# Optimization experiments

Hardware: AMD Instinct MI355X
Metric: run time of the kernel (lower is better)

## Reference

```python
import jax, jax.numpy as jnp
import numpy as np
from jax import lax

DN = ('NHWC', 'HWIO', 'NHWC')

def conv2d_same(x, W, b):
    y = lax.conv_general_dilated(x, W, window_strides=(1, 1), padding='SAME', dimension_numbers=DN)
    return y + b

def maxpool2(x):
    # 2x2 max pool, stride 2, SAME padding (NHWC)
    return lax.reduce_window(x, -jnp.inf, lax.max, (1, 2, 2, 1), (1, 2, 2, 1), 'SAME')

def setup_inputs() -> dict:
    key = jax.random.key(0)
    ks = jax.random.split(key, 6)
    B, H, W, C = 8, 64, 64, 256
    s = 0.05
    return {
        'x': jax.random.normal(ks[0], (B, H, W, C), jnp.float32),
        'Wf': jax.random.normal(ks[1], (3, 3, C, C // 8), jnp.float32) * s,
        'bf': jnp.zeros((C // 8,), jnp.float32),
        'Wg': jax.random.normal(ks[2], (3, 3, C, C // 8), jnp.float32) * s,
        'bg': jnp.zeros((C // 8,), jnp.float32),
        'Wh': jax.random.normal(ks[3], (3, 3, C, C // 2), jnp.float32) * s,
        'bh': jnp.zeros((C // 2,), jnp.float32),
        'Wo': jax.random.normal(ks[4], (1, 1, C // 2, C), jnp.float32) * s,
        'bo': jnp.zeros((C,), jnp.float32),
        'gate': jnp.ones((1,), jnp.float32),
    }

def reference(x, Wf, bf, Wg, bg, Wh, bh, Wo, bo, gate):
    B, H, W, C = x.shape
    f = maxpool2(conv2d_same(x, Wf, bf))            # [B, H/2, W/2, C//8] keys
    g = conv2d_same(x, Wg, bg)                       # [B, H, W, C//8]     queries
    h = maxpool2(conv2d_same(x, Wh, bh))            # [B, H/2, W/2, C//2] values
    N, M = H * W, (H // 2) * (W // 2)
    gq = g.reshape(B, N, C // 8)
    fk = f.reshape(B, M, C // 8)
    hv = h.reshape(B, M, C // 2)
    attn = jax.nn.softmax(jnp.einsum('bnd,bmd->bnm', gq, fk), axis=-1)  # [B, N, M]
    wo = jnp.einsum('bnm,bmv->bnv', attn, hv).reshape(B, H, W, C // 2)
    out = conv2d_same(wo, Wo, bo)                    # [B, H, W, C]
    return x + gate[0] * out
```

## Files before the change

kernel.cpp:

```cpp
#include <hip/hip_runtime.h>
#include <hip/hip_fp16.h>

constexpr int B_  = 8;
constexpr int H_  = 64;
constexpr int W_  = 64;
constexpr int C_  = 256;
constexpr int CG_ = 32;
constexpr int CH_ = 128;
constexpr int NQ_ = 4096;
constexpr int NM_ = 1024;

constexpr int GP_ = 1048576;
constexpr int HP_ = 4194304;

typedef __attribute__((ext_vector_type(8))) _Float16 half8;
typedef __attribute__((ext_vector_type(4))) _Float16 half4;
typedef __attribute__((ext_vector_type(4))) float    f32x4;

__global__ void prep_w_k(const float* __restrict__ Wg, const float* __restrict__ Wf,
                         const float* __restrict__ Wh, const float* __restrict__ Wo,
                         const float* __restrict__ bg, const float* __restrict__ bf,
                         const float* __restrict__ bh,
                         _Float16* __restrict__ Wpk, _Float16* __restrict__ Wok,
                         float* __restrict__ bc) {
    int i = blockIdx.x * 256 + threadIdx.x;
    if (i < 12 * 9 * 8 * 64 * 8) {
        int j    = i & 7;
        int lane = (i >> 3) & 63;
        int ks   = (i >> 9) & 7;
        int tap  = (i >> 12) % 9;
        int co16 = i / 36864;
        int co = co16 * 16 + (lane & 15);
        int kk = tap * 256 + ks * 32 + (lane >> 4) * 8 + j;
        float v;
        if (co < 32)      v = Wg[(size_t)kk * 32  + co];
        else if (co < 64) v = Wf[(size_t)kk * 32  + (co - 32)];
        else              v = Wh[(size_t)kk * 128 + (co - 64)];
        Wpk[i] = (_Float16)v;
        return;
    }
    int i2 = i - 12 * 9 * 8 * 64 * 8;
    if (i2 < 16 * 4 * 64 * 8) {
        int j    = i2 & 7;
        int lane = (i2 >> 3) & 63;
        int ks   = (i2 >> 9) & 3;
        int co16 = i2 >> 11;
        int co = co16 * 16 + (lane & 15);
        int k  = ks * 32 + (lane >> 4) * 8 + j;
        Wok[i2] = (_Float16)Wo[(size_t)k * 256 + co];
        return;
    }
    int co = i2 - 16 * 4 * 64 * 8;
    if (co < 192)
        bc[co] = (co < 32) ? bg[co] : (co < 64) ? bf[co - 32] : bh[co - 64];
}

__global__ __launch_bounds__(512, 4) void conv_mfma_k(
        const float* __restrict__ X, const _Float16* __restrict__ Wpk,
        const float* __restrict__ bc,
        _Float16* __restrict__ gpart, _Float16* __restrict__ fpart,
        _Float16* __restrict__ hpart) {
    __shared__ char lds[2 * 32768];
    int bid = blockIdx.x;
    int lg  = (bid & 7) * 96 + (bid >> 3);
    int ky  = lg % 3;
    int ip  = lg / 3;
    int b   = ip >> 5;
    int y0  = (ip & 31) * 2;
    int tid = threadIdx.x;
    int wid = tid >> 6;
    int rid = wid >> 2;
    int nw  = wid & 3;
    int l   = tid & 63;
    int lr  = l & 15;
    int lk  = l >> 4;

    {
#pragma unroll
        for (int j = 0; j < 8; ++j) {
            int cc  = tid + j * 512;
            int row = cc >> 11;
            int c   = cc & 2047;
            int px  = c >> 5;
            int c8  = (c & 31) * 8;
            int yin = y0 + ky - 1 + row;
            half8 v = (half8)(_Float16)0.f;
            if (yin >= 0 && yin < 64) {
                const float* s = X + (((size_t)(b * 64 + yin) * 64) + px) * 256 + c8;
                float4 a  = *reinterpret_cast<const float4*>(s);
                float4 b2 = *reinterpret_cast<const float4*>(s + 4);
                v[0] = (_Float16)a.x;  v[1] = (_Float16)a.y;
                v[2] = (_Float16)a.z;  v[3] = (_Float16)a.w;
                v[4] = (_Float16)b2.x; v[5] = (_Float16)b2.y;
                v[6] = (_Float16)b2.z; v[7] = (_Float16)b2.w;
            }
            *reinterpret_cast<half8*>(lds + row * 32768 +
                ((c * 16) ^ ((px & 7) << 4))) = v;
        }
    }
    __syncthreads();

    f32x4 acc[4][3];
#pragma unroll
    for (int mi = 0; mi < 4; ++mi)
#pragma unroll
        for (int nj = 0; nj < 3; ++nj) acc[mi][nj] = (f32x4)0.f;

    int tap0 = ky * 3;
    const char* ldsr = lds + rid * 32768;

    auto ldw = [&](int s, half8* d) {
        const _Float16* p = Wpk +
            ((((size_t)(nw * 3) * 9 + tap0 + (s >> 3)) * 8 + (s & 7)) * 64 + l) * 8;
        d[0] = *reinterpret_cast<const half8*>(p);
        d[1] = *reinterpret_cast<const half8*>(p + 36864);
        d[2] = *reinterpret_cast<const half8*>(p + 73728);
    };
    auto lda = [&](int s, half8* d) {
        int kx = s >> 3, ks = s & 7;
#pragma unroll
        for (int mi = 0; mi < 4; ++mi) {
            int px  = mi * 16 + lr + kx - 1;
            int pxc = px < 0 ? 0 : (px > 63 ? 63 : px);
            int ad  = (pxc * 512 + ks * 64 + lk * 16) ^ ((pxc & 7) << 4);
            half8 a = *reinterpret_cast<const half8*>(ldsr + ad);
            if (px < 0 || px > 63) a = (half8)(_Float16)0.f;
            d[mi] = a;
        }
    };

    half8 wb[2][3];
    half8 afb[2][4];
    ldw(0, wb[0]);
    lda(0, afb[0]);
#pragma unroll
    for (int st = 0; st < 24; ++st) {
        if (st < 23) {
            ldw(st + 1, wb[(st + 1) & 1]);
            lda(st + 1, afb[(st + 1) & 1]);
        }
        const half8* w  = wb[st & 1];
        const half8* af = afb[st & 1];
        __builtin_amdgcn_s_setprio(1);
#pragma unroll
        for (int mi = 0; mi < 4; ++mi)
            acc[mi][0] = __builtin_amdgcn_mfma_f32_16x16x32_f16(af[mi], w[0], acc[mi][0], 0, 0, 0);
#pragma unroll
        for (int mi = 0; mi < 4; ++mi)
            acc[mi][1] = __builtin_amdgcn_mfma_f32_16x16x32_f16(af[mi], w[1], acc[mi][1], 0, 0, 0);
#pragma unroll
        for (int mi = 0; mi < 4; ++mi)
            acc[mi][2] = __builtin_amdgcn_mfma_f32_16x16x32_f16(af[mi], w[2], acc[mi][2], 0, 0, 0);
        __builtin_amdgcn_s_setprio(0);
    }

    int pixbase = (b * 64 + y0 + rid) * 64;
    bool addb = (ky == 1);
#pragma unroll
    for (int nj = 0; nj < 3; ++nj) {
        int co = nw * 48 + nj * 16 + lr;
        float bias = addb ? bc[co] : 0.f;
#pragma unroll
        for (int mi = 0; mi < 4; ++mi) {
#pragma unroll
            for (int r = 0; r < 4; ++r) {
                int x = mi * 16 + lk * 4 + r;
                float v = acc[mi][nj][r] + bias;
                size_t pix = pixbase + x;
                if (co < 32)
                    gpart[(size_t)ky * GP_ + pix * 32 + co] = (_Float16)(v * 1.44269504f);
                else if (co < 64)
                    fpart[(size_t)ky * GP_ + pix * 32 + (co - 32)] = (_Float16)v;
                else
                    hpart[(size_t)ky * HP_ + pix * 128 + (co - 64)] = (_Float16)v;
            }
        }
    }
}

__global__ __launch_bounds__(256) void pools_k(const _Float16* __restrict__ fp,
                                               const _Float16* __restrict__ hp,
                                               _Float16* __restrict__ Kf,
                                               _Float16* __restrict__ Vt) {
    __shared__ float t[32][33];
    int blk = blockIdx.x;
    int tid = threadIdx.x;
    if (blk < 1024) {
        int i = blk * 256 + tid;
        int c = i & 31;
        int t2 = i >> 5;
        int px = t2 & 31;
        int py = (t2 >> 5) & 31;
        int b  = t2 >> 10;
        size_t base = (((size_t)(b * 64 + py * 2)) * 64 + px * 2) * 32 + c;
        const _Float16* p1 = fp + GP_;
        const _Float16* p2 = fp + 2 * GP_;
        auto val = [&](size_t o) { return (float)fp[o] + (float)p1[o] + (float)p2[o]; };
        float v = fmaxf(fmaxf(val(base), val(base + 32)),
                        fmaxf(val(base + 64 * 32), val(base + 64 * 32 + 32)));
        Kf[i] = (_Float16)v;
        return;
    }
    int bx = blk - 1024;
    int b  = bx >> 7;
    int kt = (bx >> 2) & 31;
    int ct = bx & 3;
    const _Float16* p1 = hp + HP_;
    const _Float16* p2 = hp + 2 * (size_t)HP_;
#pragma unroll
    for (int i = 0; i < 4; ++i) {
        int e = tid + i * 256;
        int px = e >> 5, c = e & 31;
        size_t base = (((size_t)(b * 64 + kt * 2) * 64) + px * 2) * 128 + ct * 32 + c;
        auto val = [&](size_t o) { return (float)hp[o] + (float)p1[o] + (float)p2[o]; };
        float v = fmaxf(fmaxf(val(base), val(base + 128)),
                        fmaxf(val(base + 64 * 128), val(base + 64 * 128 + 128)));
        t[px][c] = v;
    }
    __syncthreads();
#pragma unroll
    for (int i = 0; i < 4; ++i) {
        int e = tid + i * 256;
        int c = e >> 5, px = e & 31;
        Vt[((size_t)b * 128 + ct * 32 + c) * 1024 + kt * 32 + px] = (_Float16)t[px][c];
    }
}

constexpr int PP_ = 72;

__global__ __launch_bounds__(256, 2) void attn_flash_k(
        const _Float16* __restrict__ Qp,
        const _Float16* __restrict__ Kf,
        const _Float16* __restrict__ Vt,
        _Float16* __restrict__ wo) {
    __shared__ _Float16 plds[4][16][PP_];
    __shared__ _Float16 vlds[2][8192];
    int bb  = blockIdx.x >> 6;
    int qt  = blockIdx.x & 63;
    int wid = threadIdx.x >> 6;
    int l   = threadIdx.x & 63;
    int lr  = l & 15;
    int lg  = l >> 4;
    int qbase = qt * 64 + wid * 16;

    const _Float16* gp = Qp + ((size_t)bb * NQ_ + qbase + lr) * 32 + lg * 8;
    half8 bq = *reinterpret_cast<const half8*>(gp);
    bq = bq + *reinterpret_cast<const half8*>(gp + GP_);
    bq = bq + *reinterpret_cast<const half8*>(gp + 2 * GP_);

    const _Float16* Kb = Kf + (size_t)bb * NM_ * 32;
    const _Float16* Vb = Vt + (size_t)bb * 128 * NM_;

    int o0  = wid * 4096 + l * 16;
    int vr0 = o0 >> 7;
    int vc  = (o0 >> 4) & 7;
    int vsw = (vr0 & 7) << 4;
    int lsw = (lr & 7) << 4;

    f32x4 acc[8];
#pragma unroll
    for (int vt = 0; vt < 8; ++vt) acc[vt] = (f32x4)0.f;
    float m_run = -1.0e30f;
    float l_lane = 0.f;

    half8 ak0, ak1, ak2, ak3;
    f32x4 s0, s1, s2, s3;
    half4 ph0, ph1, ph2, ph3;
    float4 vst[4];

#define STAGE_LOAD(T)                                                              \
    {   const _Float16* vp = Vb + (size_t)(T) * 64 + (size_t)vr0 * NM_ + vc * 8;   \
        vst[0] = *reinterpret_cast<const float4*>(vp);                             \
        vst[1] = *reinterpret_cast<const float4*>(vp + 8 * NM_);                   \
        vst[2] = *reinterpret_cast<const float4*>(vp + 16 * NM_);                  \
        vst[3] = *reinterpret_cast<const float4*>(vp + 24 * NM_);                  \
    }

#define STAGE_WRITE(BUF)                                                           \
    {   char* vbp = (char*)vlds[BUF] + (o0 ^ vsw);                                 \
        *reinterpret_cast<float4*>(vbp)        = vst[0];                           \
        *reinterpret_cast<float4*>(vbp + 1024) = vst[1];                           \
        *reinterpret_cast<float4*>(vbp + 2048) = vst[2];                           \
        *reinterpret_cast<float4*>(vbp + 3072) = vst[3];                           \
    }

#define LOADK(T)                                                                   \
    {   const _Float16* kp = Kb + (size_t)(T) * 64 * 32;                           \
        ak0 = *reinterpret_cast<const half8*>(kp + (size_t)(lr)      * 32 + lg*8); \
        ak1 = *reinterpret_cast<const half8*>(kp + (size_t)(16 + lr) * 32 + lg*8); \
        ak2 = *reinterpret_cast<const half8*>(kp + (size_t)(32 + lr) * 32 + lg*8); \
        ak3 = *reinterpret_cast<const half8*>(kp + (size_t)(48 + lr) * 32 + lg*8); \
    }

#define QK()                                                                \
    {   __builtin_amdgcn_s_setprio(1);                                      \
        s0 = __builtin_amdgcn_mfma_f32_16x16x32_f16(ak0, bq, (f32x4)0.f, 0, 0, 0); \
        s1 = __builtin_amdgcn_mfma_f32_16x16x32_f16(ak1, bq, (f32x4)0.f, 0, 0, 0); \
        s2 = __builtin_amdgcn_mfma_f32_16x16x32_f16(ak2, bq, (f32x4)0.f, 0, 0, 0); \
        s3 = __builtin_amdgcn_mfma_f32_16x16x32_f16(ak3, bq, (f32x4)0.f, 0, 0, 0); \
        __builtin_amdgcn_s_setprio(0);                                      \
    }

#define SOFTMAX()                                                           \
    {   float lm = fmaxf(fmaxf(fmaxf(s0[0], s0[1]), fmaxf(s0[2], s0[3])),   \
                         fmaxf(fmaxf(s1[0], s1[1]), fmaxf(s1[2], s1[3])));  \
        lm = fmaxf(lm, fmaxf(fmaxf(fmaxf(s2[0], s2[1]), fmaxf(s2[2], s2[3])), \
                             fmaxf(fmaxf(s3[0], s3[1]), fmaxf(s3[2], s3[3])))); \
        if (__any(lm > m_run + 11.0f)) {                                    \
            float mx = lm;                                                  \
            mx = fmaxf(mx, __shfl_xor(mx, 16, 64));                         \
            mx = fmaxf(mx, __shfl_xor(mx, 32, 64));                         \
            float mnew  = fmaxf(m_run, mx);                                 \
            float alpha = exp2f(m_run - mnew);                              \
            l_lane *= alpha;                                                \
            _Pragma("unroll")                                               \
            for (int r = 0; r < 4; ++r) {                                   \
                float ar = __shfl(alpha, 4 * lg + r, 64);                   \
                _Pragma("unroll")                                           \
                for (int vt = 0; vt < 8; ++vt) acc[vt][r] *= ar;            \
            }                                                               \
            m_run = mnew;                                                   \
        }                                                                   \
        float ps = 0.f;                                                     \
        {   float p0 = exp2f(s0[0]-m_run), p1 = exp2f(s0[1]-m_run);         \
            float p2 = exp2f(s0[2]-m_run), p3 = exp2f(s0[3]-m_run);         \
            ps += (p0+p1)+(p2+p3);                                          \
            ph0[0]=(_Float16)p0; ph0[1]=(_Float16)p1;                       \
            ph0[2]=(_Float16)p2; ph0[3]=(_Float16)p3; }                     \
        {   float p0 = exp2f(s1[0]-m_run), p1 = exp2f(s1[1]-m_run);         \
            float p2 = exp2f(s1[2]-m_run), p3 = exp2f(s1[3]-m_run);         \
            ps += (p0+p1)+(p2+p3);                                          \
            ph1[0]=(_Float16)p0; ph1[1]=(_Float16)p1;                       \
            ph1[2]=(_Float16)p2; ph1[3]=(_Float16)p3; }                     \
        {   float p0 = exp2f(s2[0]-m_run), p1 = exp2f(s2[1]-m_run);         \
            float p2 = exp2f(s2[2]-m_run), p3 = exp2f(s2[3]-m_run);         \
            ps += (p0+p1)+(p2+p3);                                          \
            ph2[0]=(_Float16)p0; ph2[1]=(_Float16)p1;                       \
            ph2[2]=(_Float16)p2; ph2[3]=(_Float16)p3; }                     \
        {   float p0 = exp2f(s3[0]-m_run), p1 = exp2f(s3[1]-m_run);         \
            float p2 = exp2f(s3[2]-m_run), p3 = exp2f(s3[3]-m_run);         \
            ps += (p0+p1)+(p2+p3);                                          \
            ph3[0]=(_Float16)p0; ph3[1]=(_Float16)p1;                       \
            ph3[2]=(_Float16)p2; ph3[3]=(_Float16)p3; }                     \
        l_lane += ps;                                                       \
    }

#define WRITEP()                                                            \
    {   *reinterpret_cast<half4*>(&plds[wid][lr][ 0 + 4*lg]) = ph0;         \
        *reinterpret_cast<half4*>(&plds[wid][lr][16 + 4*lg]) = ph1;         \
        *reinterpret_cast<half4*>(&plds[wid][lr][32 + 4*lg]) = ph2;         \
        *reinterpret_cast<half4*>(&plds[wid][lr][48 + 4*lg]) = ph3;         \
    }

#define PV(BUF)                                                             \
    {   half8 ap0 = *reinterpret_cast<const half8*>(&plds[wid][lr][8*lg]);  \
        half8 ap1 = *reinterpret_cast<const half8*>(&plds[wid][lr][32 + 8*lg]); \
        const char* vbp = (const char*)vlds[BUF];                           \
        __builtin_amdgcn_s_setprio(1);                                      \
        _Pragma("unroll")                                                   \
        for (int vt = 0; vt < 8; ++vt) {                                    \
            int ra = (vt * 16 + lr) * 128;                                  \
            half8 bv = *reinterpret_cast<const half8*>(                     \
                vbp + ((ra + lg * 16) ^ lsw));                              \
            acc[vt] = __builtin_amdgcn_mfma_f32_16x16x32_f16(ap0, bv, acc[vt], 0, 0, 0); \
        }                                                                   \
        _Pragma("unroll")                                                   \
        for (int vt = 0; vt < 8; ++vt) {                                    \
            int ra = (vt * 16 + lr) * 128;                                  \
            half8 bv = *reinterpret_cast<const half8*>(                     \
                vbp + ((ra + (4 + lg) * 16) ^ lsw));                        \
            acc[vt] = __builtin_amdgcn_mfma_f32_16x16x32_f16(ap1, bv, acc[vt], 0, 0, 0); \
        }                                                                   \
        __builtin_amdgcn_s_setprio(0);                                      \
    }

    STAGE_LOAD(0);
    STAGE_WRITE(0);
    LOADK(0);
    __syncthreads();
    QK(); SOFTMAX();

    for (int t = 0; t < 16; ++t) {
        if (t < 15) { STAGE_LOAD(t + 1); LOADK(t + 1); }
        WRITEP();
        PV(t & 1);
        if (t < 15) STAGE_WRITE((t + 1) & 1);
        __syncthreads();
        if (t < 15) { QK(); SOFTMAX(); }
    }

#undef STAGE_LOAD
#undef STAGE_WRITE
#undef LOADK
#undef QK
#undef SOFTMAX
#undef WRITEP
#undef PV

    float lsum = l_lane;
    lsum += __shfl_xor(lsum, 16, 64);
    lsum += __shfl_xor(lsum, 32, 64);
    float inv = 1.f / lsum;
#pragma unroll
    for (int r = 0; r < 4; ++r) {
        float ir = __shfl(inv, 4 * lg + r, 64);
        _Float16* orow = wo + ((size_t)bb * NQ_ + qbase + 4 * lg + r) * 128 + lr;
#pragma unroll
        for (int vt = 0; vt < 8; ++vt) orow[vt * 16] = (_Float16)(acc[vt][r] * ir);
    }
}

__global__ __launch_bounds__(256, 2) void conv1x1_mfma_k(
        const _Float16* __restrict__ wo, const _Float16* __restrict__ Wok,
        const float* __restrict__ bo, const float* __restrict__ X,
        const float* __restrict__ gate, float* __restrict__ out) {
    __shared__ char lds[64 * 256];
    int pix0 = blockIdx.x * 64;
    int tid = threadIdx.x;
    int wq = tid >> 6;
    int l  = tid & 63;
    int lr = l & 15;
    int lg = l >> 4;

    {
        const float4* sp = reinterpret_cast<const float4*>(wo + (size_t)pix0 * 128);
#pragma unroll
        for (int j = 0; j < 4; ++j) {
            int c = tid + j * 256;
            int px = c >> 4;
            *reinterpret_cast<float4*>(lds + ((c * 16) ^ ((px & 7) << 4))) = sp[c];
        }
    }
    __syncthreads();

    f32x4 acc[4][4];
#pragma unroll
    for (int mi = 0; mi < 4; ++mi)
#pragma unroll
        for (int nj = 0; nj < 4; ++nj) acc[mi][nj] = (f32x4)0.f;

#pragma unroll
    for (int ks = 0; ks < 4; ++ks) {
        half8 ap[4];
#pragma unroll
        for (int mi = 0; mi < 4; ++mi) {
            int px = mi * 16 + lr;
            int ad = (px * 256 + ks * 64 + lg * 16) ^ ((px & 7) << 4);
            ap[mi] = *reinterpret_cast<const half8*>(lds + ad);
        }
#pragma unroll
        for (int nj = 0; nj < 4; ++nj) {
            int co16 = wq * 4 + nj;
            half8 bv = *reinterpret_cast<const half8*>(
                Wok + (((size_t)co16 * 4 + ks) * 64 + l) * 8);
#pragma unroll
            for (int mi = 0; mi < 4; ++mi)
                acc[mi][nj] = __builtin_amdgcn_mfma_f32_16x16x32_f16(ap[mi], bv, acc[mi][nj], 0, 0, 0);
        }
    }

    float gt = gate[0];
#pragma unroll
    for (int nj = 0; nj < 4; ++nj) {
        int co = wq * 64 + nj * 16 + lr;
        float bias = bo[co];
#pragma unroll
        for (int mi = 0; mi < 4; ++mi) {
#pragma unroll
            for (int r = 0; r < 4; ++r) {
                size_t o = (size_t)(pix0 + mi * 16 + lg * 4 + r) * 256 + co;
                out[o] = X[o] + gt * (acc[mi][nj][r] + bias);
            }
        }
    }
}

extern "C" void kernel_launch(void* const* d_in, const int* in_sizes, int n_in,
                              void* d_out, int out_size, void* d_ws, size_t ws_size,
                              hipStream_t stream) {
    const float* X    = (const float*)d_in[0];
    const float* Wf   = (const float*)d_in[1];
    const float* bf   = (const float*)d_in[2];
    const float* Wg   = (const float*)d_in[3];
    const float* bg   = (const float*)d_in[4];
    const float* Wh   = (const float*)d_in[5];
    const float* bh   = (const float*)d_in[6];
    const float* Wo   = (const float*)d_in[7];
    const float* bo   = (const float*)d_in[8];
    const float* gate = (const float*)d_in[9];
    float* out = (float*)d_out;

    _Float16* gpart = (_Float16*)d_ws;
    _Float16* fpart = gpart + 3 * (size_t)GP_;
    _Float16* hpart = fpart + 3 * (size_t)GP_;
    _Float16* Kf    = hpart + 3 * (size_t)HP_;
    _Float16* Vt    = Kf + 262144;
    _Float16* Wpk   = Vt + 1048576;
    float*    bc    = (float*)(Wpk + 442368);
    _Float16* Wok   = (_Float16*)(bc + 192);
    _Float16* wobuf = hpart;

    prep_w_k<<<(12*9*8*64*8 + 16*4*64*8 + 192 + 255) / 256, 256, 0, stream>>>(
        Wg, Wf, Wh, Wo, bg, bf, bh, Wpk, Wok, bc);
    conv_mfma_k<<<3 * B_ * 32, 512, 0, stream>>>(X, Wpk, bc, gpart, fpart, hpart);
    pools_k<<<2048, 256, 0, stream>>>(fpart, hpart, Kf, Vt);
    attn_flash_k<<<B_ * 64, 256, 0, stream>>>(gpart, Kf, Vt, wobuf);
    conv1x1_mfma_k<<<(B_ * NQ_) / 64, 256, 0, stream>>>(wobuf, Wok, bo, X, gate, out);
}
```

Before: 107.7 us.

## Pre-pad input to fp16 buffer and shrink conv tiles to half-row blocks

Adds a prep pass that converts X to a zero-padded fp16 NHWC buffer, so the conv kernel copies raw fp16 data into LDS without per-element conversion or boundary masking. The conv kernel now handles one half-row (32 pixels) per 256-thread block instead of two full rows per 512-thread block, with smaller LDS and accumulator footprint, four times as many blocks, and higher occupancy bounds. The explicit software double-buffering of weight and activation loads and the setprio hints are removed. The cost is an extra full pass writing and reading the padded fp16 copy of X, and each weight fragment is now reused across fewer pixels.

```diff
diff --git a/kernel.cpp b/kernel.cpp
--- a/kernel.cpp
+++ b/kernel.cpp
@@ -9,38 +9,65 @@
 constexpr int CH_ = 128;
 constexpr int NQ_ = 4096;
 constexpr int NM_ = 1024;
+constexpr int XP_ = 66;
 
 constexpr int GP_ = 1048576;
 constexpr int HP_ = 4194304;
+
+constexpr int NWPK_ = 12 * 9 * 8 * 64 * 8;
+constexpr int NWOK_ = 16 * 4 * 64 * 8;
+constexpr int NXC_  = B_ * XP_ * XP_ * 32;
 
 typedef __attribute__((ext_vector_type(8))) _Float16 half8;
 typedef __attribute__((ext_vector_type(4))) _Float16 half4;
 typedef __attribute__((ext_vector_type(4))) float    f32x4;
 
-__global__ void prep_w_k(const float* __restrict__ Wg, const float* __restrict__ Wf,
-                         const float* __restrict__ Wh, const float* __restrict__ Wo,
-                         const float* __restrict__ bg, const float* __restrict__ bf,
-                         const float* __restrict__ bh,
-                         _Float16* __restrict__ Wpk, _Float16* __restrict__ Wok,
-                         float* __restrict__ bc) {
+__global__ void prep_all_k(const float* __restrict__ X,
+                           const float* __restrict__ Wg, const float* __restrict__ Wf,
+                           const float* __restrict__ Wh, const float* __restrict__ Wo,
+                           const float* __restrict__ bg, const float* __restrict__ bf,
+                           const float* __restrict__ bh,
+                           _Float16* __restrict__ Xpad, _Float16* __restrict__ Wpk,
+                           _Float16* __restrict__ Wok, float* __restrict__ bc) {
     int i = blockIdx.x * 256 + threadIdx.x;
-    if (i < 12 * 9 * 8 * 64 * 8) {
-        int j    = i & 7;
-        int lane = (i >> 3) & 63;
-        int ks   = (i >> 9) & 7;
-        int tap  = (i >> 12) % 9;
-        int co16 = i / 36864;
+    if (i < NXC_) {
+        int c8 = i & 31;
+        int px = i >> 5;
+        int xx = px % XP_;
+        int t  = px / XP_;
+        int yy = t % XP_;
+        int b  = t / XP_;
+        half8 v = (half8)(_Float16)0.f;
+        if (yy >= 1 && yy <= 64 && xx >= 1 && xx <= 64) {
+            const float* s = X + (((size_t)(b * 64 + yy - 1) * 64) + (xx - 1)) * 256 + c8 * 8;
+            float4 a  = *reinterpret_cast<const float4*>(s);
+            float4 b2 = *reinterpret_cast<const float4*>(s + 4);
+            v[0] = (_Float16)a.x;  v[1] = (_Float16)a.y;
+            v[2] = (_Float16)a.z;  v[3] = (_Float16)a.w;
+            v[4] = (_Float16)b2.x; v[5] = (_Float16)b2.y;
+            v[6] = (_Float16)b2.z; v[7] = (_Float16)b2.w;
+        }
+        *reinterpret_cast<half8*>(Xpad + (size_t)i * 8) = v;
+        return;
+    }
+    int iw = i - NXC_;
+    if (iw < NWPK_) {
+        int j    = iw & 7;
+        int lane = (iw >> 3) & 63;
+        int ks   = (iw >> 9) & 7;
+        int tap  = (iw >> 12) % 9;
+        int co16 = iw / 36864;
         int co = co16 * 16 + (lane & 15);
         int kk = tap * 256 + ks * 32 + (lane >> 4) * 8 + j;
         float v;
         if (co < 32)      v = Wg[(size_t)kk * 32  + co];
         else if (co < 64) v = Wf[(size_t)kk * 32  + (co - 32)];
         else              v = Wh[(size_t)kk * 128 + (co - 64)];
-        Wpk[i] = (_Float16)v;
+        Wpk[iw] = (_Float16)v;
         return;
     }
-    int i2 = i - 12 * 9 * 8 * 64 * 8;
-    if (i2 < 16 * 4 * 64 * 8) {
+    int i2 = iw - NWPK_;
+    if (i2 < NWOK_) {
         int j    = i2 & 7;
         int lane = (i2 >> 3) & 63;
         int ks   = (i2 >> 9) & 3;
@@ -50,123 +77,87 @@
         Wok[i2] = (_Float16)Wo[(size_t)k * 256 + co];
         return;
     }
-    int co = i2 - 16 * 4 * 64 * 8;
+    int co = i2 - NWOK_;
     if (co < 192)
         bc[co] = (co < 32) ? bg[co] : (co < 64) ? bf[co - 32] : bh[co - 64];
 }
 
-__global__ __launch_bounds__(512, 4) void conv_mfma_k(
-        const float* __restrict__ X, const _Float16* __restrict__ Wpk,
+__global__ __launch_bounds__(256, 8) void conv_mfma_k(
+        const _Float16* __restrict__ Xpad, const _Float16* __restrict__ Wpk,
         const float* __restrict__ bc,
         _Float16* __restrict__ gpart, _Float16* __restrict__ fpart,
         _Float16* __restrict__ hpart) {
-    __shared__ char lds[2 * 32768];
+    __shared__ char lds[34 * 512];
     int bid = blockIdx.x;
-    int lg  = (bid & 7) * 96 + (bid >> 3);
+    int lg  = (bid & 7) * 384 + (bid >> 3);
     int ky  = lg % 3;
-    int ip  = lg / 3;
-    int b   = ip >> 5;
-    int y0  = (ip & 31) * 2;
+    int t   = lg / 3;
+    int xh  = t & 1;
+    int y   = (t >> 1) & 63;
+    int b   = t >> 7;
     int tid = threadIdx.x;
-    int wid = tid >> 6;
-    int rid = wid >> 2;
-    int nw  = wid & 3;
+    int nw  = tid >> 6;
     int l   = tid & 63;
     int lr  = l & 15;
     int lk  = l >> 4;
 
     {
-#pragma unroll
-        for (int j = 0; j < 8; ++j) {
-            int cc  = tid + j * 512;
-            int row = cc >> 11;
-            int c   = cc & 2047;
-            int px  = c >> 5;
-            int c8  = (c & 31) * 8;
-            int yin = y0 + ky - 1 + row;
-            half8 v = (half8)(_Float16)0.f;
-            if (yin >= 0 && yin < 64) {
-                const float* s = X + (((size_t)(b * 64 + yin) * 64) + px) * 256 + c8;
-                float4 a  = *reinterpret_cast<const float4*>(s);
-                float4 b2 = *reinterpret_cast<const float4*>(s + 4);
-                v[0] = (_Float16)a.x;  v[1] = (_Float16)a.y;
-                v[2] = (_Float16)a.z;  v[3] = (_Float16)a.w;
-                v[4] = (_Float16)b2.x; v[5] = (_Float16)b2.y;
-                v[6] = (_Float16)b2.z; v[7] = (_Float16)b2.w;
-            }
-            *reinterpret_cast<half8*>(lds + row * 32768 +
-                ((c * 16) ^ ((px & 7) << 4))) = v;
+        const float4* src = reinterpret_cast<const float4*>(
+            Xpad + (((size_t)(b * XP_ + y + ky) * XP_) + xh * 32) * 256);
+        for (int c = tid; c < 34 * 32; c += 256) {
+            int q = c >> 5;
+            float4 v = src[c];
+            *reinterpret_cast<float4*>(lds + ((c * 16) ^ ((q & 7) << 4))) = v;
         }
     }
     __syncthreads();
 
-    f32x4 acc[4][3];
-#pragma unroll
-    for (int mi = 0; mi < 4; ++mi)
+    f32x4 acc[2][3];
+#pragma unroll
+    for (int mi = 0; mi < 2; ++mi)
 #pragma unroll
         for (int nj = 0; nj < 3; ++nj) acc[mi][nj] = (f32x4)0.f;
 
     int tap0 = ky * 3;
-    const char* ldsr = lds + rid * 32768;
-
-    auto ldw = [&](int s, half8* d) {
-        const _Float16* p = Wpk +
-            ((((size_t)(nw * 3) * 9 + tap0 + (s >> 3)) * 8 + (s & 7)) * 64 + l) * 8;
-        d[0] = *reinterpret_cast<const half8*>(p);
-        d[1] = *reinterpret_cast<const half8*>(p + 36864);
-        d[2] = *reinterpret_cast<const half8*>(p + 73728);
-    };
-    auto lda = [&](int s, half8* d) {
-        int kx = s >> 3, ks = s & 7;
-#pragma unroll
-        for (int mi = 0; mi < 4; ++mi) {
-            int px  = mi * 16 + lr + kx - 1;
-            int pxc = px < 0 ? 0 : (px > 63 ? 63 : px);
-            int ad  = (pxc * 512 + ks * 64 + lk * 16) ^ ((pxc & 7) << 4);
-            half8 a = *reinterpret_cast<const half8*>(ldsr + ad);
-            if (px < 0 || px > 63) a = (half8)(_Float16)0.f;
-            d[mi] = a;
-        }
-    };
-
-    half8 wb[2][3];
-    half8 afb[2][4];
-    ldw(0, wb[0]);
-    lda(0, afb[0]);
 #pragma unroll
     for (int st = 0; st < 24; ++st) {
-        if (st < 23) {
-            ldw(st + 1, wb[(st + 1) & 1]);
-            lda(st + 1, afb[(st + 1) & 1]);
-        }
-        const half8* w  = wb[st & 1];
-        const half8* af = afb[st & 1];
-        __builtin_amdgcn_s_setprio(1);
-#pragma unroll
-        for (int mi = 0; mi < 4; ++mi)
-            acc[mi][0] = __builtin_amdgcn_mfma_f32_16x16x32_f16(af[mi], w[0], acc[mi][0], 0, 0, 0);
-#pragma unroll
-        for (int mi = 0; mi < 4; ++mi)
-            acc[mi][1] = __builtin_amdgcn_mfma_f32_16x16x32_f16(af[mi], w[1], acc[mi][1], 0, 0, 0);
-#pragma unroll
-        for (int mi = 0; mi < 4; ++mi)
-            acc[mi][2] = __builtin_amdgcn_mfma_f32_16x16x32_f16(af[mi], w[2], acc[mi][2], 0, 0, 0);
-        __builtin_amdgcn_s_setprio(0);
-    }
-
-    int pixbase = (b * 64 + y0 + rid) * 64;
+        int kx = st >> 3, ks = st & 7;
+        const _Float16* wp = Wpk +
+            ((((size_t)(nw * 3) * 9 + tap0 + kx) * 8 + ks) * 64 + l) * 8;
+        half8 w0 = *reinterpret_cast<const half8*>(wp);
+        half8 w1 = *reinterpret_cast<const half8*>(wp + 36864);
+        half8 w2 = *reinterpret_cast<const half8*>(wp + 73728);
+        half8 af[2];
+#pragma unroll
+        for (int mi = 0; mi < 2; ++mi) {
+            int q  = mi * 16 + lr + kx;
+            int ad = (q * 512 + ks * 64 + lk * 16) ^ ((q & 7) << 4);
+            af[mi] = *reinterpret_cast<const half8*>(lds + ad);
+        }
+#pragma unroll
+        for (int mi = 0; mi < 2; ++mi)
+            acc[mi][0] = __builtin_amdgcn_mfma_f32_16x16x32_f16(af[mi], w0, acc[mi][0], 0, 0, 0);
+#pragma unroll
+        for (int mi = 0; mi < 2; ++mi)
+            acc[mi][1] = __builtin_amdgcn_mfma_f32_16x16x32_f16(af[mi], w1, acc[mi][1], 0, 0, 0);
+#pragma unroll
+        for (int mi = 0; mi < 2; ++mi)
+            acc[mi][2] = __builtin_amdgcn_mfma_f32_16x16x32_f16(af[mi], w2, acc[mi][2], 0, 0, 0);
+    }
+
+    int pixbase = (b * 64 + y) * 64 + xh * 32;
     bool addb = (ky == 1);
 #pragma unroll
     for (int nj = 0; nj < 3; ++nj) {
         int co = nw * 48 + nj * 16 + lr;
         float bias = addb ? bc[co] : 0.f;
 #pragma unroll
-        for (int mi = 0; mi < 4; ++mi) {
+        for (int mi = 0; mi < 2; ++mi) {
 #pragma unroll
             for (int r = 0; r < 4; ++r) {
-                int x = mi * 16 + lk * 4 + r;
+                int px = mi * 16 + lk * 4 + r;
                 float v = acc[mi][nj][r] + bias;
-                size_t pix = pixbase + x;
+                size_t pix = pixbase + px;
                 if (co < 32)
                     gpart[(size_t)ky * GP_ + pix * 32 + co] = (_Float16)(v * 1.44269504f);
                 else if (co < 64)
@@ -496,13 +487,15 @@
     _Float16* Kf    = hpart + 3 * (size_t)HP_;
     _Float16* Vt    = Kf + 262144;
     _Float16* Wpk   = Vt + 1048576;
-    float*    bc    = (float*)(Wpk + 442368);
+    float*    bc    = (float*)(Wpk + 589824);
     _Float16* Wok   = (_Float16*)(bc + 192);
+    _Float16* Xpad  = Wok + 32768;
     _Float16* wobuf = hpart;
 
-    prep_w_k<<<(12*9*8*64*8 + 16*4*64*8 + 192 + 255) / 256, 256, 0, stream>>>(
-        Wg, Wf, Wh, Wo, bg, bf, bh, Wpk, Wok, bc);
-    conv_mfma_k<<<3 * B_ * 32, 512, 0, stream>>>(X, Wpk, bc, gpart, fpart, hpart);
+    int prep_n = NXC_ + NWPK_ + NWOK_ + 192;
+    prep_all_k<<<(prep_n + 255) / 256, 256, 0, stream>>>(
+        X, Wg, Wf, Wh, Wo, bg, bf, bh, Xpad, Wpk, Wok, bc);
+    conv_mfma_k<<<3 * B_ * 64 * 2, 256, 0, stream>>>(Xpad, Wpk, bc, gpart, fpart, hpart);
     pools_k<<<2048, 256, 0, stream>>>(fpart, hpart, Kf, Vt);
     attn_flash_k<<<B_ * 64, 256, 0, stream>>>(gpart, Kf, Vt, wobuf);
     conv1x1_mfma_k<<<(B_ * NQ_) / 64, 256, 0, stream>>>(wobuf, Wok, bo, X, gate, out);
```

Result: slower. 118.4 us (+9.9%).
